# Kernel optimization log

Hardware: AMD Instinct MI355X
Metric: run time of the kernel (lower is better)

The kernel has to match this reference:

```python
import jax, jax.numpy as jnp
import numpy as np
import math

D_MODEL = 2048
NUM_HEADS = 16
QUERY_GROUPS = 4
HEAD_DIM = D_MODEL // NUM_HEADS  # 128
B, T = 2, 2048


def setup_inputs() -> dict:
    key = jax.random.key(0)
    ks = jax.random.split(key, 9)
    s = 0.02
    return {
        "x": jax.random.normal(ks[0], (B, T, D_MODEL), dtype=jnp.float32),
        "Wq": jax.random.normal(ks[1], (D_MODEL, NUM_HEADS * HEAD_DIM), dtype=jnp.float32) * s,
        "bq": jnp.zeros((NUM_HEADS * HEAD_DIM,), dtype=jnp.float32),
        "Wk": jax.random.normal(ks[2], (D_MODEL, QUERY_GROUPS * HEAD_DIM), dtype=jnp.float32) * s,
        "bk": jnp.zeros((QUERY_GROUPS * HEAD_DIM,), dtype=jnp.float32),
        "Wv": jax.random.normal(ks[3], (D_MODEL, QUERY_GROUPS * HEAD_DIM), dtype=jnp.float32) * s,
        "bv": jnp.zeros((QUERY_GROUPS * HEAD_DIM,), dtype=jnp.float32),
        "Wo": jax.random.normal(ks[4], (D_MODEL, D_MODEL), dtype=jnp.float32) * s,
        "bo": jnp.zeros((D_MODEL,), dtype=jnp.float32),
    }


def reference(x, Wq, bq, Wk, bk, Wv, bv, Wo, bo):
    Bb, Tt, Dd = x.shape
    G, H, hd = QUERY_GROUPS, NUM_HEADS, HEAD_DIM
    m = H // G  # heads per group
    # projections
    q = (x @ Wq + bq).reshape(Bb, Tt, G, m, hd)   # [B,T,G,m,hd]
    k = (x @ Wk + bk).reshape(Bb, Tt, G, hd)      # [B,T,G,hd]
    v = (x @ Wv + bv).reshape(Bb, Tt, G, hd)
    # scores with native group broadcast (no explicit K/V expansion)
    scores = jnp.einsum('btgmd,bsgd->bgmts', q, k) / math.sqrt(hd)  # [B,G,m,T,T]
    p = jax.nn.softmax(scores, axis=-1)
    out = jnp.einsum('bgmts,bsgd->btgmd', p, v).reshape(Bb, Tt, Dd)
    # output projection (dropout is identity in eval / p=0)
    return out @ Wo + bo
```

## Files before the change

### kernel.cpp

```cpp
#include <hip/hip_runtime.h>

#define D_MODEL 2048
#define T_SEQ   2048
#define NBATCH  2
#define NH      16
#define NG      4
#define HD      128
#define NQKV    3072

typedef short bf16x8 __attribute__((ext_vector_type(8)));
typedef float f32x4  __attribute__((ext_vector_type(4)));
typedef float f32x16 __attribute__((ext_vector_type(16)));
typedef short s16x4  __attribute__((ext_vector_type(4)));

__device__ __forceinline__ short f2bf(float f) {
  union { float f; unsigned u; } v; v.f = f;
  unsigned r = v.u + 0x7fffu + ((v.u >> 16) & 1u);
  return (short)(r >> 16);
}

__device__ __forceinline__ float bf2f(short s) {
  union { unsigned u; float f; } v; v.u = ((unsigned)(unsigned short)s) << 16;
  return v.f;
}

__device__ __forceinline__ float fast_exp2(float x) {
#if __has_builtin(__builtin_amdgcn_exp2f)
  return __builtin_amdgcn_exp2f(x);
#else
  return __expf(x * 0.6931471805599453f);
#endif
}

__device__ __forceinline__ unsigned cvt_pk_bf16(float a, float b) {
  unsigned r;
  asm("v_cvt_pk_bf16_f32 %0, %1, %2" : "=v"(r) : "v"(a), "v"(b));
  return r;
}

__device__ __forceinline__ void gload16(const void* g, void* l) {
  __builtin_amdgcn_global_load_lds(
      (const __attribute__((address_space(1))) void*)g,
      (__attribute__((address_space(3))) void*)l, 16, 0, 0);
}

__global__ __launch_bounds__(256) void convert_x_kernel(
    const float* __restrict__ x, short* __restrict__ o, int n) {
  int i = (blockIdx.x * 256 + threadIdx.x) * 4;
  if (i >= n) return;
  float4 v = *(const float4*)(x + i);
  s16x4 s;
  s[0] = f2bf(v.x); s[1] = f2bf(v.y); s[2] = f2bf(v.z); s[3] = f2bf(v.w);
  *(s16x4*)(o + i) = s;
}

__global__ __launch_bounds__(256) void wtrans_kernel(
    const float* __restrict__ W, short* __restrict__ dst,
    int K, int N, int rowOff, int dstStride) {
  __shared__ float t[32][33];
  int tx = threadIdx.x & 31, ty = threadIdx.x >> 5;
  int kb = blockIdx.x * 32, nb = blockIdx.y * 32;
#pragma unroll
  for (int i = 0; i < 4; ++i)
    t[ty + 8*i][tx] = W[(long)(kb + ty + 8*i) * N + nb + tx];
  __syncthreads();
#pragma unroll
  for (int i = 0; i < 4; ++i)
    dst[(long)(rowOff + nb + ty + 8*i) * dstStride + kb + tx] = f2bf(t[tx][ty + 8*i]);
}

__global__ __launch_bounds__(256) void vtrans_kernel(
    const short* __restrict__ qkv, short* __restrict__ vt) {
  __shared__ short t[32][33];
  int bg = blockIdx.z; int b = bg >> 2, g = bg & 3;
  int sb = blockIdx.x * 32, db = blockIdx.y * 32;
  int tx = threadIdx.x & 31, ty = threadIdx.x >> 5;
  const short* src = qkv + (long)(b * T_SEQ) * NQKV + D_MODEL + NG * HD + g * HD;
#pragma unroll
  for (int i = 0; i < 4; ++i)
    t[ty + 8*i][tx] = src[(long)(sb + ty + 8*i) * NQKV + db + tx];
  __syncthreads();
  short* dst = vt + ((long)bg * HD + db) * T_SEQ + sb;
#pragma unroll
  for (int i = 0; i < 4; ++i)
    dst[(long)(ty + 8*i) * T_SEQ + tx] = t[tx][ty + 8*i];
}

__global__ __launch_bounds__(256) void gemm_kernel(
    const short* __restrict__ A, const short* __restrict__ BT,
    const float* __restrict__ b0, const float* __restrict__ b1, const float* __restrict__ b2,
    void* __restrict__ Cout, int M, int N, int K, int mode) {
  __shared__ __align__(16) short As[128 * 64];
  __shared__ __align__(16) short Bs[128 * 64];
  const int tid = threadIdx.x;
  const int w = tid >> 6, lane = tid & 63;
  const int l15 = lane & 15, quad = lane >> 4;
  const int wr = w & 1, wc = w >> 1;
  const int nb = blockIdx.x, mb = blockIdx.y;
  const short* Ab = A + (long)mb * 128 * K;
  const short* Bb = BT + (long)nb * 128 * K;

  f32x4 acc[4][4];
#pragma unroll
  for (int i = 0; i < 4; ++i)
#pragma unroll
    for (int j = 0; j < 4; ++j) acc[i][j] = 0.0f;

  for (int k0 = 0; k0 < K; k0 += 64) {
    __syncthreads();
#pragma unroll
    for (int t = 0; t < 4; ++t) {
      int chunk = w * 256 + t * 64 + lane;
      int r = chunk >> 3, c = chunk & 7;
      int gc = c ^ (r & 7);
      gload16(Ab + (long)r * K + k0 + gc * 8, As + (w * 256 + t * 64) * 8);
      gload16(Bb + (long)r * K + k0 + gc * 8, Bs + (w * 256 + t * 64) * 8);
    }
    __syncthreads();
#pragma unroll
    for (int ks = 0; ks < 2; ++ks) {
      bf16x8 af[4], bfr[4];
#pragma unroll
      for (int i = 0; i < 4; ++i) {
        int r = wr * 64 + i * 16 + l15;
        af[i] = *(const bf16x8*)(As + r * 64 + (((ks * 4 + quad) ^ (r & 7)) * 8));
      }
#pragma unroll
      for (int j = 0; j < 4; ++j) {
        int r = wc * 64 + j * 16 + l15;
        bfr[j] = *(const bf16x8*)(Bs + r * 64 + (((ks * 4 + quad) ^ (r & 7)) * 8));
      }
#pragma unroll
      for (int i = 0; i < 4; ++i)
#pragma unroll
        for (int j = 0; j < 4; ++j)
          acc[i][j] = __builtin_amdgcn_mfma_f32_16x16x32_bf16(af[i], bfr[j], acc[i][j], 0, 0, 0);
    }
  }

  float biasv[4];
#pragma unroll
  for (int j = 0; j < 4; ++j) {
    int col = nb * 128 + wc * 64 + j * 16 + l15;
    float bv;
    if (mode == 0) {
      if (col < 2048)      bv = b0[col];
      else if (col < 2560) bv = b1[col - 2048];
      else                 bv = b2[col - 2560];
    } else bv = b0[col];
    biasv[j] = bv;
  }
  if (mode == 0) {
    short* C = (short*)Cout;
#pragma unroll
    for (int i = 0; i < 4; ++i)
#pragma unroll
      for (int j = 0; j < 4; ++j)
#pragma unroll
        for (int r = 0; r < 4; ++r) {
          int row = mb * 128 + wr * 64 + i * 16 + quad * 4 + r;
          int col = nb * 128 + wc * 64 + j * 16 + l15;
          C[(long)row * N + col] = f2bf(acc[i][j][r] + biasv[j]);
        }
  } else {
    float* C = (float*)Cout;
#pragma unroll
    for (int i = 0; i < 4; ++i)
#pragma unroll
      for (int j = 0; j < 4; ++j)
#pragma unroll
        for (int r = 0; r < 4; ++r) {
          int row = mb * 128 + wr * 64 + i * 16 + quad * 4 + r;
          int col = nb * 128 + wc * 64 + j * 16 + l15;
          C[(long)row * N + col] = acc[i][j][r] + biasv[j];
        }
  }
}

__global__ __launch_bounds__(256, 2) void attn_kernel(
    const short* __restrict__ qkv, const short* __restrict__ vt,
    short* __restrict__ aout) {
  __shared__ __align__(16) short smem[16384];
  short* Ks = smem;
  short* Vs = smem + 8192;

  const int tid = threadIdx.x;
  const int w = tid >> 6, lane = tid & 63;
  const int l31 = lane & 31, hi = lane >> 5;
  const int qt = blockIdx.x, h = blockIdx.y, b = blockIdx.z;
  const int g = h >> 2;
  const short* qbase = qkv + (long)(b * T_SEQ + qt * 128) * NQKV + h * HD;
  const short* kbase = qkv + (long)(b * T_SEQ) * NQKV + D_MODEL + g * HD;
  const short* vbase = vt + (long)(b * NG + g) * HD * T_SEQ;
  const float QSCALE = 0.08838834764831845f * 1.4426950408889634f;

  int kroff[4], vroff[4], dst[4];
#pragma unroll
  for (int t = 0; t < 4; ++t) {
    int chunk = w * 256 + t * 64 + lane;
    { int r = chunk >> 4, c = chunk & 15, gc = c ^ (r & 15);
      kroff[t] = r * NQKV + gc * 8; }
    { int r = chunk >> 3, c = chunk & 7, gc = c ^ (r & 7);
      vroff[t] = r * T_SEQ + gc * 8; }
    dst[t] = chunk * 8;
  }

  bf16x8 qfrag[8];
  {
    const short* qrow = qbase + (long)(w * 32 + l31) * NQKV + hi * 8;
#pragma unroll
    for (int ks = 0; ks < 8; ++ks) {
      bf16x8 v = *(const bf16x8*)(qrow + ks * 16);
#pragma unroll
      for (int e = 0; e < 8; ++e) v[e] = f2bf(bf2f(v[e]) * QSCALE);
      qfrag[ks] = v;
    }
  }

#pragma unroll
  for (int t = 0; t < 4; ++t) {
    gload16(kbase + kroff[t], Ks + dst[t]);
    gload16(vbase + vroff[t], Vs + dst[t]);
  }

  f32x16 oaccT[4];
#pragma unroll
  for (int i = 0; i < 4; ++i) oaccT[i] = 0.0f;
  float lpart[4] = {0.f, 0.f, 0.f, 0.f};

  __syncthreads();

  bf16x8 kpre[4], vpre[4];
  for (int st = 0; st < T_SEQ / 64; ++st) {
    const bool pf = (st + 1 < T_SEQ / 64);
    if (pf) {
      const short* kb2 = kbase + (long)(st + 1) * 64 * NQKV;
      const short* vb2 = vbase + (st + 1) * 64;
#pragma unroll
      for (int t = 0; t < 4; ++t) {
        kpre[t] = *(const bf16x8*)(kb2 + kroff[t]);
        vpre[t] = *(const bf16x8*)(vb2 + vroff[t]);
      }
    }

    f32x16 sacc[2];
    sacc[0] = 0.0f; sacc[1] = 0.0f;
    __builtin_amdgcn_s_setprio(1);
#pragma unroll
    for (int ks = 0; ks < 8; ++ks) {
#pragma unroll
      for (int sb = 0; sb < 2; ++sb) {
        int srow = sb * 32 + l31;
        bf16x8 a = *(const bf16x8*)(Ks + srow * 128 + (((ks * 2 + hi) ^ (srow & 15)) * 8));
        sacc[sb] = __builtin_amdgcn_mfma_f32_32x32x16_bf16(a, qfrag[ks], sacc[sb], 0, 0, 0);
      }
    }
    __builtin_amdgcn_s_setprio(0);

    float p0[16], p1[16];
#pragma unroll
    for (int r = 0; r < 16; ++r) p0[r] = fast_exp2(sacc[0][r]);
#pragma unroll
    for (int r = 0; r < 16; ++r) p1[r] = fast_exp2(sacc[1][r]);
#pragma unroll
    for (int r = 0; r < 16; ++r) lpart[r & 3] += p0[r] + p1[r];

    __builtin_amdgcn_s_setprio(1);
#pragma unroll
    for (int k2 = 0; k2 < 4; ++k2) {
      const float* pp = (k2 & 2) ? p1 : p0;
      const int bo = (k2 & 1) * 8;
      unsigned Pa = cvt_pk_bf16(pp[bo + 0], pp[bo + 1]);
      unsigned Pb = cvt_pk_bf16(pp[bo + 2], pp[bo + 3]);
      unsigned Pc = cvt_pk_bf16(pp[bo + 4], pp[bo + 5]);
      unsigned Pd = cvt_pk_bf16(pp[bo + 6], pp[bo + 7]);
      unsigned ta = __shfl_xor(Pa, 32);
      unsigned tb = __shfl_xor(Pb, 32);
      unsigned tc = __shfl_xor(Pc, 32);
      unsigned td = __shfl_xor(Pd, 32);
      unsigned w0 = hi ? tc : Pa;
      unsigned w1 = hi ? td : Pb;
      unsigned w2 = hi ? Pc : ta;
      unsigned w3 = hi ? Pd : tb;
      union { unsigned u[4]; bf16x8 v; } pfr;
      pfr.u[0] = w0; pfr.u[1] = w1; pfr.u[2] = w2; pfr.u[3] = w3;
#pragma unroll
      for (int db = 0; db < 4; ++db) {
        int drow = db * 32 + l31;
        bf16x8 a = *(const bf16x8*)(Vs + drow * 64 + (((k2 * 2 + hi) ^ (drow & 7)) * 8));
        oaccT[db] = __builtin_amdgcn_mfma_f32_32x32x16_bf16(a, pfr.v, oaccT[db], 0, 0, 0);
      }
    }
    __builtin_amdgcn_s_setprio(0);

    __syncthreads();
    if (pf) {
#pragma unroll
      for (int t = 0; t < 4; ++t) {
        *(bf16x8*)(Ks + dst[t]) = kpre[t];
        *(bf16x8*)(Vs + dst[t]) = vpre[t];
      }
    }
    __syncthreads();
  }

  float lsum = (lpart[0] + lpart[1]) + (lpart[2] + lpart[3]);
  float lfull = lsum + __shfl_xor(lsum, 32);
  float inv = 1.0f / lfull;

  short* Osm = smem;
  const int qrl = w * 32 + l31;
#pragma unroll
  for (int db = 0; db < 4; ++db)
#pragma unroll
    for (int r = 0; r < 16; ++r) {
      int dloc = (r & 3) + 8 * (r >> 2) + 4 * hi;
      int d = db * 32 + dloc;
      int c = d >> 3;
      Osm[qrl * 128 + ((c ^ (qrl & 15)) * 8) + (d & 7)] = f2bf(oaccT[db][r] * inv);
    }
  __syncthreads();

  short* obase = aout + (long)(b * T_SEQ + qt * 128) * D_MODEL + h * HD;
  const int row = tid >> 1, ch = tid & 1;
#pragma unroll
  for (int j = 0; j < 8; ++j) {
    int c2 = ch * 8 + j;
    bf16x8 v = *(const bf16x8*)(Osm + row * 128 + ((c2 ^ (row & 15)) * 8));
    *(bf16x8*)(obase + (long)row * D_MODEL + c2 * 8) = v;
  }
}

extern "C" void kernel_launch(void* const* d_in, const int* in_sizes, int n_in,
                              void* d_out, int out_size, void* d_ws, size_t ws_size,
                              hipStream_t stream) {
  const float* x  = (const float*)d_in[0];
  const float* Wq = (const float*)d_in[1];
  const float* bq = (const float*)d_in[2];
  const float* Wk = (const float*)d_in[3];
  const float* bk = (const float*)d_in[4];
  const float* Wv = (const float*)d_in[5];
  const float* bv = (const float*)d_in[6];
  const float* Wo = (const float*)d_in[7];
  const float* bo = (const float*)d_in[8];

  const long NTOK = (long)NBATCH * T_SEQ;
  short* xb    = (short*)d_ws;
  short* wqkvT = xb + NTOK * D_MODEL;
  short* woT   = wqkvT + (long)NQKV * D_MODEL;
  short* qkvb  = woT + (long)D_MODEL * D_MODEL;
  short* vtb   = qkvb + NTOK * NQKV;
  short* attnb = vtb + (long)NBATCH * NG * HD * T_SEQ;

  int nX = (int)(NTOK * D_MODEL);
  convert_x_kernel<<<nX / (256 * 4), 256, 0, stream>>>(x, xb, nX);
  wtrans_kernel<<<dim3(D_MODEL / 32, D_MODEL / 32), 256, 0, stream>>>(Wq, wqkvT, D_MODEL, D_MODEL, 0, D_MODEL);
  wtrans_kernel<<<dim3(D_MODEL / 32, 512 / 32), 256, 0, stream>>>(Wk, wqkvT, D_MODEL, 512, 2048, D_MODEL);
  wtrans_kernel<<<dim3(D_MODEL / 32, 512 / 32), 256, 0, stream>>>(Wv, wqkvT, D_MODEL, 512, 2560, D_MODEL);
  wtrans_kernel<<<dim3(D_MODEL / 32, D_MODEL / 32), 256, 0, stream>>>(Wo, woT, D_MODEL, D_MODEL, 0, D_MODEL);

  gemm_kernel<<<dim3(NQKV / 128, NTOK / 128), 256, 0, stream>>>(
      xb, wqkvT, bq, bk, bv, (void*)qkvb, (int)NTOK, NQKV, D_MODEL, 0);

  vtrans_kernel<<<dim3(T_SEQ / 32, HD / 32, NBATCH * NG), 256, 0, stream>>>(qkvb, vtb);

  attn_kernel<<<dim3(T_SEQ / 128, NH, NBATCH), 256, 0, stream>>>(qkvb, vtb, attnb);

  gemm_kernel<<<dim3(D_MODEL / 128, NTOK / 128), 256, 0, stream>>>(
      attnb, woT, bo, bo, bo, (void*)d_out, (int)NTOK, D_MODEL, D_MODEL, 1);
}
```

Before: 335.9 us.

## Double-buffer K/V LDS tiles, split QK accumulators, use permlane32 swap

```diff
diff --git a/kernel.cpp b/kernel.cpp
--- a/kernel.cpp
+++ b/kernel.cpp
@@ -12,6 +12,7 @@
 typedef float f32x4  __attribute__((ext_vector_type(4)));
 typedef float f32x16 __attribute__((ext_vector_type(16)));
 typedef short s16x4  __attribute__((ext_vector_type(4)));
+typedef unsigned u32x4 __attribute__((ext_vector_type(4)));
 
 __device__ __forceinline__ short f2bf(float f) {
   union { float f; unsigned u; } v; v.f = f;
@@ -36,6 +37,10 @@
   unsigned r;
   asm("v_cvt_pk_bf16_f32 %0, %1, %2" : "=v"(r) : "v"(a), "v"(b));
   return r;
+}
+
+__device__ __forceinline__ void permlane32_swap(unsigned &a, unsigned &b) {
+  asm("v_permlane32_swap_b32 %0, %1" : "+v"(a), "+v"(b));
 }
 
 __device__ __forceinline__ void gload16(const void* g, void* l) {
@@ -180,9 +185,7 @@
 __global__ __launch_bounds__(256, 2) void attn_kernel(
     const short* __restrict__ qkv, const short* __restrict__ vt,
     short* __restrict__ aout) {
-  __shared__ __align__(16) short smem[16384];
-  short* Ks = smem;
-  short* Vs = smem + 8192;
+  __shared__ __align__(16) short smem[32768];
 
   const int tid = threadIdx.x;
   const int w = tid >> 6, lane = tid & 63;
@@ -219,8 +222,8 @@
 
 #pragma unroll
   for (int t = 0; t < 4; ++t) {
-    gload16(kbase + kroff[t], Ks + dst[t]);
-    gload16(vbase + vroff[t], Vs + dst[t]);
+    gload16(kbase + kroff[t], smem + dst[t]);
+    gload16(vbase + vroff[t], smem + 8192 + dst[t]);
   }
 
   f32x16 oaccT[4];
@@ -230,9 +233,12 @@
 
   __syncthreads();
 
+  int cur = 0;
   bf16x8 kpre[4], vpre[4];
   for (int st = 0; st < T_SEQ / 64; ++st) {
     const bool pf = (st + 1 < T_SEQ / 64);
+    short* Ks = smem + cur * 16384;
+    short* Vs = Ks + 8192;
     if (pf) {
       const short* kb2 = kbase + (long)(st + 1) * 64 * NQKV;
       const short* vb2 = vbase + (st + 1) * 64;
@@ -243,8 +249,8 @@
       }
     }
 
-    f32x16 sacc[2];
-    sacc[0] = 0.0f; sacc[1] = 0.0f;
+    f32x16 sacc[2][2];
+    sacc[0][0] = 0.0f; sacc[0][1] = 0.0f; sacc[1][0] = 0.0f; sacc[1][1] = 0.0f;
     __builtin_amdgcn_s_setprio(1);
 #pragma unroll
     for (int ks = 0; ks < 8; ++ks) {
@@ -252,16 +258,16 @@
       for (int sb = 0; sb < 2; ++sb) {
         int srow = sb * 32 + l31;
         bf16x8 a = *(const bf16x8*)(Ks + srow * 128 + (((ks * 2 + hi) ^ (srow & 15)) * 8));
-        sacc[sb] = __builtin_amdgcn_mfma_f32_32x32x16_bf16(a, qfrag[ks], sacc[sb], 0, 0, 0);
+        sacc[sb][ks & 1] = __builtin_amdgcn_mfma_f32_32x32x16_bf16(a, qfrag[ks], sacc[sb][ks & 1], 0, 0, 0);
       }
     }
     __builtin_amdgcn_s_setprio(0);
 
     float p0[16], p1[16];
 #pragma unroll
-    for (int r = 0; r < 16; ++r) p0[r] = fast_exp2(sacc[0][r]);
-#pragma unroll
-    for (int r = 0; r < 16; ++r) p1[r] = fast_exp2(sacc[1][r]);
+    for (int r = 0; r < 16; ++r) p0[r] = fast_exp2(sacc[0][0][r] + sacc[0][1][r]);
+#pragma unroll
+    for (int r = 0; r < 16; ++r) p1[r] = fast_exp2(sacc[1][0][r] + sacc[1][1][r]);
 #pragma unroll
     for (int r = 0; r < 16; ++r) lpart[r & 3] += p0[r] + p1[r];
 
@@ -274,34 +280,30 @@
       unsigned Pb = cvt_pk_bf16(pp[bo + 2], pp[bo + 3]);
       unsigned Pc = cvt_pk_bf16(pp[bo + 4], pp[bo + 5]);
       unsigned Pd = cvt_pk_bf16(pp[bo + 6], pp[bo + 7]);
-      unsigned ta = __shfl_xor(Pa, 32);
-      unsigned tb = __shfl_xor(Pb, 32);
-      unsigned tc = __shfl_xor(Pc, 32);
-      unsigned td = __shfl_xor(Pd, 32);
-      unsigned w0 = hi ? tc : Pa;
-      unsigned w1 = hi ? td : Pb;
-      unsigned w2 = hi ? Pc : ta;
-      unsigned w3 = hi ? Pd : tb;
-      union { unsigned u[4]; bf16x8 v; } pfr;
-      pfr.u[0] = w0; pfr.u[1] = w1; pfr.u[2] = w2; pfr.u[3] = w3;
+      permlane32_swap(Pa, Pc);
+      permlane32_swap(Pb, Pd);
+      u32x4 pu; pu[0] = Pa; pu[1] = Pb; pu[2] = Pc; pu[3] = Pd;
+      bf16x8 pfr = __builtin_bit_cast(bf16x8, pu);
 #pragma unroll
       for (int db = 0; db < 4; ++db) {
         int drow = db * 32 + l31;
         bf16x8 a = *(const bf16x8*)(Vs + drow * 64 + (((k2 * 2 + hi) ^ (drow & 7)) * 8));
-        oaccT[db] = __builtin_amdgcn_mfma_f32_32x32x16_bf16(a, pfr.v, oaccT[db], 0, 0, 0);
+        oaccT[db] = __builtin_amdgcn_mfma_f32_32x32x16_bf16(a, pfr, oaccT[db], 0, 0, 0);
       }
     }
     __builtin_amdgcn_s_setprio(0);
 
+    if (pf) {
+      short* Kn = smem + (cur ^ 1) * 16384;
+      short* Vn = Kn + 8192;
+#pragma unroll
+      for (int t = 0; t < 4; ++t) {
+        *(bf16x8*)(Kn + dst[t]) = kpre[t];
+        *(bf16x8*)(Vn + dst[t]) = vpre[t];
+      }
+    }
     __syncthreads();
-    if (pf) {
-#pragma unroll
-      for (int t = 0; t < 4; ++t) {
-        *(bf16x8*)(Ks + dst[t]) = kpre[t];
-        *(bf16x8*)(Vs + dst[t]) = vpre[t];
-      }
-    }
-    __syncthreads();
+    cur ^= 1;
   }
 
   float lsum = (lpart[0] + lpart[1]) + (lpart[2] + lpart[3]);
```

Result: no change. 334.2 us (-0.5%).
